# Optimization experiments

Hardware: AMD Instinct MI355X
Metric: run time of the kernel (lower is better)

The kernel has to match this reference:

```python
import jax, jax.numpy as jnp
import numpy as np

N = 100000      # nodes (10000 graphs of 10 nodes)
E = 1600000     # directed edges
IN, H1, H2, H3 = 128, 128, 128, 64
L1, L2, FINAL = 512, 256, 8
K = 2


def lrelu(x, slope):
    return jnp.where(x >= 0, x, slope * x)


def _with_self_loops(edge_index, n):
    loop = jnp.arange(n, dtype=edge_index.dtype)
    src = jnp.concatenate([edge_index[0], loop])
    dst = jnp.concatenate([edge_index[1], loop])
    return src, dst


def _gcn_norm(src, dst, n):
    # symmetric normalization deg^-1/2[src] * deg^-1/2[dst] (self-loops included)
    deg = jax.ops.segment_sum(jnp.ones_like(src, dtype=jnp.float32), dst, num_segments=n)
    dinv = jnp.where(deg > 0, jax.lax.rsqrt(deg), 0.0)
    return dinv[src] * dinv[dst]


def sgconv(x, src, dst, norm, W, b, k_hops):
    # SGConv: K rounds of normalized sparse propagation, then linear
    for _ in range(k_hops):
        x = jax.ops.segment_sum(norm[:, None] * x[src], dst, num_segments=x.shape[0])
    return x @ W + b


def gatconv(x, src, dst, W, att_src, att_dst, b):
    # single-head PyG GATConv (lin bias=False, negative_slope=0.2, self-loops)
    n = x.shape[0]
    h = x @ W                                   # [N, H3]
    a_s = h @ att_src                           # [N]
    a_d = h @ att_dst                           # [N]
    e = lrelu(a_s[src] + a_d[dst], 0.2)         # [E+N]
    m = jax.ops.segment_max(e, dst, num_segments=n)
    e = jnp.exp(e - m[dst])
    s = jax.ops.segment_sum(e, dst, num_segments=n)
    alpha = e / s[dst]
    out = jax.ops.segment_sum(alpha[:, None] * h[src], dst, num_segments=n)
    return out + b


def setup_inputs() -> dict:
    key = jax.random.key(0)
    ks = jax.random.split(key, 16)

    def w(k, shape, fan_in):
        return (jax.random.normal(k, shape, jnp.float32) / np.sqrt(fan_in)).astype(jnp.float32)

    return {
        "x": jax.random.normal(ks[0], (N, IN), jnp.float32),
        "edge_index": jax.random.randint(ks[1], (2, E), 0, N),
        "W1": w(ks[2], (IN, H1), IN), "b1": jnp.zeros((H1,), jnp.float32),
        "W2": w(ks[3], (H1, H2), H1), "b2": jnp.zeros((H2,), jnp.float32),
        "Wg": w(ks[4], (H2, H3), H2),
        "att_src": w(ks[5], (H3,), H3), "att_dst": w(ks[6], (H3,), H3),
        "bg": jnp.zeros((H3,), jnp.float32),
        "Wl1": w(ks[7], (10 * H3, L1), 10 * H3), "bl1": jnp.zeros((L1,), jnp.float32),
        "Wl2": w(ks[8], (L1, L2), L1), "bl2": jnp.zeros((L2,), jnp.float32),
        "Wl3": w(ks[9], (L2, FINAL), L2), "bl3": jnp.zeros((FINAL,), jnp.float32),
    }


def reference(x, edge_index, W1, b1, W2, b2, Wg, att_src, att_dst, bg,
              Wl1, bl1, Wl2, bl2, Wl3, bl3):
    n = x.shape[0]
    src, dst = _with_self_loops(edge_index, n)
    norm = _gcn_norm(src, dst, n)

    h = sgconv(x, src, dst, norm, W1, b1, K)       # conv1
    h = lrelu(h, 0.1)                              # dropout is identity in eval mode
    h = lrelu(sgconv(h, src, dst, norm, W2, b2, K), 0.1)
    h = lrelu(gatconv(h, src, dst, Wg, att_src, att_dst, bg), 0.1)

    h = h.reshape(n // 10, 10 * H3)                # group 10 nodes per graph
    h = lrelu(h @ Wl1 + bl1, 0.1)
    h = lrelu(h @ Wl2 + bl2, 0.1)
    return h @ Wl3 + bl3
```

## Files before the change

kernel.cpp:

```cpp
#include <hip/hip_runtime.h>

typedef __attribute__((ext_vector_type(8))) short short8;
typedef __attribute__((ext_vector_type(8))) unsigned short ushort8;
typedef __attribute__((ext_vector_type(4))) float floatx4;
typedef __attribute__((ext_vector_type(2))) float floatx2;

#define NBQ  1024
#define NBLK 128

__device__ __forceinline__ float bf2f(unsigned short u) {
    union { unsigned u; float f; } v; v.u = ((unsigned)u) << 16; return v.f;
}
__device__ __forceinline__ float bflo(unsigned u) {
    union { unsigned u; float f; } v; v.u = u << 16; return v.f;
}
__device__ __forceinline__ float bfhi(unsigned u) {
    union { unsigned u; float f; } v; v.u = u & 0xFFFF0000u; return v.f;
}
__device__ __forceinline__ unsigned short f2bf(float f) {
    union { float f; unsigned u; } v; v.f = f;
    unsigned r = v.u + 0x7FFFu + ((v.u >> 16) & 1u);
    return (unsigned short)(r >> 16);
}
__device__ __forceinline__ unsigned pack2bf(float a, float b) {
    return (unsigned)f2bf(a) | ((unsigned)f2bf(b) << 16);
}
__device__ __forceinline__ float lrelu(float x, float s) { return x >= 0.f ? x : s * x; }

#define PK_FP8_LO(a, b, old) __builtin_amdgcn_cvt_pk_fp8_f32((a), (b), (old), false)
#define PK_FP8_HI(a, b, old) __builtin_amdgcn_cvt_pk_fp8_f32((a), (b), (old), true)
#define UPK_FP8_LO(u)        __builtin_amdgcn_cvt_pk_f32_fp8((int)(u), false)
#define UPK_FP8_HI(u)        __builtin_amdgcn_cvt_pk_f32_fp8((int)(u), true)

__global__ __launch_bounds__(256) void cast_scale8(const float* __restrict__ in, const float* __restrict__ dinv,
                                                   unsigned* __restrict__ outp, int nquads) {
    int i = blockIdx.x * 256 + threadIdx.x;
    if (i < nquads) {
        float s = dinv[i >> 5];
        float4 v = *(const float4*)(in + 4 * (size_t)i);
        int w = PK_FP8_LO(v.x * s, v.y * s, 0);
        w = PK_FP8_HI(v.z * s, v.w * s, w);
        outp[i] = (unsigned)w;
    }
}

__global__ __launch_bounds__(256) void cast_bf2fp8(const uint2* __restrict__ in, unsigned* __restrict__ outp,
                                                   int nquads) {
    int i = blockIdx.x * 256 + threadIdx.x;
    if (i < nquads) {
        uint2 v = in[i];
        int w = PK_FP8_LO(bflo(v.x), bfhi(v.x), 0);
        w = PK_FP8_HI(bflo(v.y), bfhi(v.y), w);
        outp[i] = (unsigned)w;
    }
}

__global__ __launch_bounds__(256) void wcast(const float* __restrict__ w0, const float* __restrict__ w1,
                                             const float* __restrict__ w2, const float* __restrict__ w3,
                                             const float* __restrict__ w4, unsigned* __restrict__ outp,
                                             int c0, int c1, int c2, int c3, int c4) {
    int i = blockIdx.x * 256 + threadIdx.x;
    if (i >= c4) return;
    const float* src; int base;
    if      (i < c0) { src = w0; base = 0;  }
    else if (i < c1) { src = w1; base = c0; }
    else if (i < c2) { src = w2; base = c1; }
    else if (i < c3) { src = w3; base = c2; }
    else             { src = w4; base = c3; }
    float2 v = *(const float2*)(src + 2 * (size_t)(i - base));
    outp[i] = pack2bf(v.x, v.y);
}

__global__ __launch_bounds__(256) void hist_k(const int* __restrict__ dst, int* __restrict__ cnt,
                                              int e, int et, int nb) {
    __shared__ int h[NBQ];
    for (int i = threadIdx.x; i < nb; i += 256) h[i] = 0;
    __syncthreads();
    int chunk = (et + NBLK - 1) / NBLK;
    int c0 = blockIdx.x * chunk;
    int c1 = c0 + chunk < et ? c0 + chunk : et;
    for (int i = c0 + (int)threadIdx.x; i < c1; i += 256) {
        int d = (i < e) ? dst[i] : (i - e);
        atomicAdd(&h[d >> 7], 1);
    }
    __syncthreads();
    for (int i = threadIdx.x; i < nb; i += 256) cnt[blockIdx.x * NBQ + i] = h[i];
}

__global__ __launch_bounds__(256) void btot_k(const int* __restrict__ cnt, int* __restrict__ btot, int nb) {
    int b = blockIdx.x * 256 + threadIdx.x;
    if (b >= nb) return;
    int s = 0;
    for (int blk = 0; blk < NBLK; ++blk) s += cnt[blk * NBQ + b];
    btot[b] = s;
}

__global__ __launch_bounds__(256) void bscan_k(const int* __restrict__ btot, int* __restrict__ bbase,
                                               int nb, int et) {
    __shared__ int sd[256];
    int t = threadIdx.x;
    int i0 = t * 4;
    int loc[4]; int s = 0;
    for (int j = 0; j < 4; ++j) { int i = i0 + j; loc[j] = (i < nb) ? btot[i] : 0; s += loc[j]; }
    sd[t] = s; __syncthreads();
    for (int off = 1; off < 256; off <<= 1) {
        int v = (t >= off) ? sd[t - off] : 0;
        __syncthreads();
        sd[t] += v;
        __syncthreads();
    }
    int run = sd[t] - s;
    for (int j = 0; j < 4; ++j) {
        int i = i0 + j;
        if (i < nb) { bbase[i] = run; run += loc[j]; }
    }
    if (t == 255) bbase[nb] = et;
}

__global__ __launch_bounds__(256) void scan_cnt(int* __restrict__ cnt, const int* __restrict__ bbase,
                                                int nb) {
    int b = blockIdx.x * 256 + threadIdx.x;
    if (b >= nb) return;
    int base = bbase[b];
    for (int blk = 0; blk < NBLK; ++blk) {
        int* p = &cnt[blk * NBQ + b];
        int t = *p; *p = base; base += t;
    }
}

__global__ __launch_bounds__(256) void scatter_k(const int* __restrict__ src, const int* __restrict__ dst,
                                                 const int* __restrict__ cnt,
                                                 int* __restrict__ ebuf, int e, int et, int nb) {
    __shared__ int cur[NBQ];
    for (int i = threadIdx.x; i < nb; i += 256) cur[i] = cnt[blockIdx.x * NBQ + i];
    __syncthreads();
    int chunk = (et + NBLK - 1) / NBLK;
    int c0 = blockIdx.x * chunk;
    int c1 = c0 + chunk < et ? c0 + chunk : et;
    for (int i = c0 + (int)threadIdx.x; i < c1; i += 256) {
        int s, d;
        if (i < e) { s = src[i]; d = dst[i]; }
        else       { s = d = i - e; }
        int pos = atomicAdd(&cur[d >> 7], 1);
        ebuf[pos] = s | ((d & 127) << 17);
    }
}

__global__ __launch_bounds__(256) void finalize_k(const int* __restrict__ ebuf, const int* __restrict__ bbase,
                                                  int* __restrict__ offsets, float* __restrict__ dinv,
                                                  int* __restrict__ csr_s, int n, int et) {
    __shared__ int ldeg[128];
    __shared__ int lscan[128];
    __shared__ int cur[128];
    int b = blockIdx.x;
    int n0 = b << 7;
    if (threadIdx.x < 128) ldeg[threadIdx.x] = 0;
    __syncthreads();
    int e0 = bbase[b], e1 = bbase[b + 1];
    for (int i = e0 + (int)threadIdx.x; i < e1; i += 256)
        atomicAdd(&ldeg[(ebuf[i] >> 17) & 127], 1);
    __syncthreads();
    if (threadIdx.x < 128) lscan[threadIdx.x] = ldeg[threadIdx.x];
    __syncthreads();
    for (int off = 1; off < 128; off <<= 1) {
        int v = 0;
        if (threadIdx.x < 128 && (int)threadIdx.x >= off) v = lscan[threadIdx.x - off];
        __syncthreads();
        if (threadIdx.x < 128) lscan[threadIdx.x] += v;
        __syncthreads();
    }
    if (threadIdx.x < 128) {
        int base = e0 + lscan[threadIdx.x] - ldeg[threadIdx.x];
        cur[threadIdx.x] = base;
        int node = n0 + threadIdx.x;
        if (node < n) {
            offsets[node] = base;
            dinv[node] = rsqrtf((float)ldeg[threadIdx.x]);
        }
    }
    if (b == 0 && threadIdx.x == 0) offsets[n] = et;
    __syncthreads();
    for (int i = e0 + (int)threadIdx.x; i < e1; i += 256) {
        int ent = ebuf[i];
        int pos = atomicAdd(&cur[(ent >> 17) & 127], 1);
        csr_s[pos] = ent & 0x1FFFF;
    }
}


#define ACC16F(u) { floatx2 t0_ = UPK_FP8_LO((u).x), t1_ = UPK_FP8_HI((u).x); \
                    a[0] += t0_.x; a[1] += t0_.y; a[2] += t1_.x; a[3] += t1_.y; \
                    t0_ = UPK_FP8_LO((u).y); t1_ = UPK_FP8_HI((u).y); \
                    a[4] += t0_.x; a[5] += t0_.y; a[6] += t1_.x; a[7] += t1_.y; \
                    t0_ = UPK_FP8_LO((u).z); t1_ = UPK_FP8_HI((u).z); \
                    a[8] += t0_.x; a[9] += t0_.y; a[10] += t1_.x; a[11] += t1_.y; \
                    t0_ = UPK_FP8_LO((u).w); t1_ = UPK_FP8_HI((u).w); \
                    a[12] += t0_.x; a[13] += t0_.y; a[14] += t1_.x; a[15] += t1_.y; }

__global__ __launch_bounds__(256) void prop8_kernel(const uint4* __restrict__ xin, const int* __restrict__ offs,
                                                    const int* __restrict__ csr_s, const float* __restrict__ dinv,
                                                    int sq, int out8f, uint4* __restrict__ out8,
                                                    uint4* __restrict__ out16, int n) {
    int node = blockIdx.x * 32 + (threadIdx.x >> 3);
    if (node >= n) return;
    int li = threadIdx.x & 7;
    int beg = offs[node], end = offs[node + 1];
    float a[16];
#pragma unroll
    for (int j = 0; j < 16; ++j) a[j] = 0.f;
    int e = beg;
    for (; e + 1 < end; e += 2) {
        int s0 = csr_s[e];
        int s1 = csr_s[e + 1];
        uint4 u0 = xin[(size_t)s0 * 8 + li];
        uint4 u1 = xin[(size_t)s1 * 8 + li];
        ACC16F(u0); ACC16F(u1);
    }
    if (e < end) {
        int s = csr_s[e];
        uint4 u = xin[(size_t)s * 8 + li];
        ACC16F(u);
    }
    float f = dinv[node];
    if (sq) f *= f;
    if (out8f) {
        int w0 = PK_FP8_LO(a[0] * f, a[1] * f, 0);   w0 = PK_FP8_HI(a[2] * f, a[3] * f, w0);
        int w1 = PK_FP8_LO(a[4] * f, a[5] * f, 0);   w1 = PK_FP8_HI(a[6] * f, a[7] * f, w1);
        int w2 = PK_FP8_LO(a[8] * f, a[9] * f, 0);   w2 = PK_FP8_HI(a[10] * f, a[11] * f, w2);
        int w3 = PK_FP8_LO(a[12] * f, a[13] * f, 0); w3 = PK_FP8_HI(a[14] * f, a[15] * f, w3);
        uint4 o; o.x = (unsigned)w0; o.y = (unsigned)w1; o.z = (unsigned)w2; o.w = (unsigned)w3;
        out8[(size_t)node * 8 + li] = o;
    } else {
        uint4 o1, o2;
        o1.x = pack2bf(a[0] * f, a[1] * f);   o1.y = pack2bf(a[2] * f, a[3] * f);
        o1.z = pack2bf(a[4] * f, a[5] * f);   o1.w = pack2bf(a[6] * f, a[7] * f);
        o2.x = pack2bf(a[8] * f, a[9] * f);   o2.y = pack2bf(a[10] * f, a[11] * f);
        o2.z = pack2bf(a[12] * f, a[13] * f); o2.w = pack2bf(a[14] * f, a[15] * f);
        out16[(size_t)node * 16 + li * 2]     = o1;
        out16[(size_t)node * 16 + li * 2 + 1] = o2;
    }
}


__global__ __launch_bounds__(256) void gemm_mfma(const unsigned short* __restrict__ A,
                                                 const unsigned short* __restrict__ Bw,
                                                 const float* __restrict__ bias, unsigned short* __restrict__ C,
                                                 const float* __restrict__ oscale,
                                                 const float* __restrict__ attS, const float* __restrict__ attD,
                                                 float* __restrict__ oas, float* __restrict__ oad,
                                                 int M, int K, int Nc, float slope, int act) {
    __shared__ __align__(16) unsigned short As[64 * 40];
    __shared__ __align__(16) unsigned short Bs[64 * 40];
    const int tid  = threadIdx.x;
    const int wave = tid >> 6;
    const int lane = tid & 63;
    const int q    = lane >> 4;
    const int r16  = lane & 15;
    const int m0 = blockIdx.x * 64;
    const int n0 = blockIdx.y * 64;

    floatx4 acc0 = {0.f,0.f,0.f,0.f}, acc1 = acc0, acc2 = acc0, acc3 = acc0;

    const int am = tid >> 2;
    const int ak = (tid & 3) * 8;
    const int bk = tid >> 3;
    const int bn = (tid & 7) * 8;
    const int gm = m0 + am;

    ushort8 sva, svb;
    if (gm < M) sva = *(const ushort8*)(A + (size_t)gm * K + ak);
    else        for (int j = 0; j < 8; ++j) sva[j] = 0;
    svb = *(const ushort8*)(Bw + (size_t)bk * Nc + n0 + bn);

    for (int k0 = 0; k0 < K; k0 += 32) {
        *(ushort8*)(&As[am * 40 + ak]) = sva;
        for (int j = 0; j < 8; ++j) Bs[(bn + j) * 40 + bk] = svb[j];
        __syncthreads();
        if (k0 + 32 < K) {
            if (gm < M) sva = *(const ushort8*)(A + (size_t)gm * K + k0 + 32 + ak);
            svb = *(const ushort8*)(Bw + (size_t)(k0 + 32 + bk) * Nc + n0 + bn);
        }
        short8 bfrag = *(const short8*)(&Bs[(wave * 16 + r16) * 40 + q * 8]);
        short8 a0 = *(const short8*)(&As[(r16) * 40 + q * 8]);
        short8 a1 = *(const short8*)(&As[(16 + r16) * 40 + q * 8]);
        short8 a2 = *(const short8*)(&As[(32 + r16) * 40 + q * 8]);
        short8 a3 = *(const short8*)(&As[(48 + r16) * 40 + q * 8]);
        acc0 = __builtin_amdgcn_mfma_f32_16x16x32_bf16(a0, bfrag, acc0, 0, 0, 0);
        acc1 = __builtin_amdgcn_mfma_f32_16x16x32_bf16(a1, bfrag, acc1, 0, 0, 0);
        acc2 = __builtin_amdgcn_mfma_f32_16x16x32_bf16(a2, bfrag, acc2, 0, 0, 0);
        acc3 = __builtin_amdgcn_mfma_f32_16x16x32_bf16(a3, bfrag, acc3, 0, 0, 0);
        __syncthreads();
    }
    int cn = n0 + wave * 16 + r16;
    float bv = bias ? bias[cn] : 0.f;
    floatx4 aa[4] = {acc0, acc1, acc2, acc3};
    float ps[16], pd[16];
    float avs = attS ? attS[cn] : 0.f;
    float avd = attS ? attD[cn] : 0.f;
    for (int ms = 0; ms < 4; ++ms)
        for (int rr = 0; rr < 4; ++rr) {
            int cm = m0 + ms * 16 + q * 4 + rr;
            float v = aa[ms][rr] + bv;
            if (act) v = lrelu(v, slope);
            if (oscale && cm < M) v *= oscale[cm];
            if (cm < M) C[(size_t)cm * Nc + cn] = f2bf(v);
            ps[ms * 4 + rr] = v * avs;
            pd[ms * 4 + rr] = v * avd;
        }
    if (attS) {
        for (int off = 1; off < 16; off <<= 1)
#pragma unroll
            for (int i = 0; i < 16; ++i) {
                ps[i] += __shfl_xor(ps[i], off, 64);
                pd[i] += __shfl_xor(pd[i], off, 64);
            }
        float* sd = (float*)As;
        if (tid < 128) sd[tid] = 0.f;
        __syncthreads();
        if (r16 == 0) {
#pragma unroll
            for (int i = 0; i < 16; ++i) {
                int row = (i >> 2) * 16 + q * 4 + (i & 3);
                atomicAdd(&sd[row], ps[i]);
                atomicAdd(&sd[64 + row], pd[i]);
            }
        }
        __syncthreads();
        if (tid < 64 && m0 + tid < M) {
            oas[m0 + tid] = sd[tid];
            oad[m0 + tid] = sd[64 + tid];
        }
    }
}

__global__ __launch_bounds__(256) void gat_agg(const uint4* __restrict__ hg, const float* __restrict__ a_s,
                                               const float* __restrict__ a_d, const int* __restrict__ offs,
                                               const int* __restrict__ csr_s, const float* __restrict__ bg,
                                               uint4* __restrict__ out, int n) {
    int node = blockIdx.x * 32 + (threadIdx.x >> 3);
    if (node >= n) return;
    int li = threadIdx.x & 7;
    int beg = offs[node], end = offs[node + 1];
    float ad = a_d[node];
    float a0=0.f,a1=0.f,a2=0.f,a3=0.f,a4=0.f,a5=0.f,a6=0.f,a7=0.f, ssum=0.f;
    int e = beg;
    for (; e + 1 < end; e += 2) {
        int s0 = csr_s[e];
        int s1 = csr_s[e + 1];
        float t0 = a_s[s0] + ad;
        float t1 = a_s[s1] + ad;
        uint4 u0 = hg[(size_t)s0 * 8 + li];
        uint4 u1 = hg[(size_t)s1 * 8 + li];
        t0 = t0 < 0.f ? 0.2f * t0 : t0;
        t1 = t1 < 0.f ? 0.2f * t1 : t1;
        float w0 = __expf(t0);
        float w1 = __expf(t1);
        ssum += w0 + w1;
        a0 = fmaf(w0, bflo(u0.x), a0); a1 = fmaf(w0, bfhi(u0.x), a1);
        a2 = fmaf(w0, bflo(u0.y), a2); a3 = fmaf(w0, bfhi(u0.y), a3);
        a4 = fmaf(w0, bflo(u0.z), a4); a5 = fmaf(w0, bfhi(u0.z), a5);
        a6 = fmaf(w0, bflo(u0.w), a6); a7 = fmaf(w0, bfhi(u0.w), a7);
        a0 = fmaf(w1, bflo(u1.x), a0); a1 = fmaf(w1, bfhi(u1.x), a1);
        a2 = fmaf(w1, bflo(u1.y), a2); a3 = fmaf(w1, bfhi(u1.y), a3);
        a4 = fmaf(w1, bflo(u1.z), a4); a5 = fmaf(w1, bfhi(u1.z), a5);
        a6 = fmaf(w1, bflo(u1.w), a6); a7 = fmaf(w1, bfhi(u1.w), a7);
    }
    if (e < end) {
        int s0 = csr_s[e];
        float t0 = a_s[s0] + ad;
        uint4 u0 = hg[(size_t)s0 * 8 + li];
        t0 = t0 < 0.f ? 0.2f * t0 : t0;
        float w0 = __expf(t0);
        ssum += w0;
        a0 = fmaf(w0, bflo(u0.x), a0); a1 = fmaf(w0, bfhi(u0.x), a1);
        a2 = fmaf(w0, bflo(u0.y), a2); a3 = fmaf(w0, bfhi(u0.y), a3);
        a4 = fmaf(w0, bflo(u0.z), a4); a5 = fmaf(w0, bfhi(u0.z), a5);
        a6 = fmaf(w0, bflo(u0.w), a6); a7 = fmaf(w0, bfhi(u0.w), a7);
    }
    float inv = 1.0f / ssum;
    int f0 = li * 8;
    uint4 o;
    o.x = pack2bf(lrelu(a0 * inv + bg[f0 + 0], 0.1f), lrelu(a1 * inv + bg[f0 + 1], 0.1f));
    o.y = pack2bf(lrelu(a2 * inv + bg[f0 + 2], 0.1f), lrelu(a3 * inv + bg[f0 + 3], 0.1f));
    o.z = pack2bf(lrelu(a4 * inv + bg[f0 + 4], 0.1f), lrelu(a5 * inv + bg[f0 + 5], 0.1f));
    o.w = pack2bf(lrelu(a6 * inv + bg[f0 + 6], 0.1f), lrelu(a7 * inv + bg[f0 + 7], 0.1f));
    out[(size_t)node * 8 + li] = o;
}


__global__ __launch_bounds__(256) void final_gemm(const unsigned short* __restrict__ m2, const float* __restrict__ W3,
                                                  const float* __restrict__ b3,
                                                  float* __restrict__ out, int ng) {
    int idx = blockIdx.x * 256 + threadIdx.x;
    if (idx >= ng * 8) return;
    int r = idx >> 3, c = idx & 7;
    float acc = b3[c];
    const unsigned short* row = m2 + (size_t)r * 256;
    for (int k = 0; k < 256; ++k) acc = fmaf(bf2f(row[k]), W3[k * 8 + c], acc);
    out[idx] = acc;
}


extern "C" void kernel_launch(void* const* d_in, const int* in_sizes, int n_in,
                              void* d_out, int out_size, void* d_ws, size_t ws_size,
                              hipStream_t stream) {
    const int N  = in_sizes[0] / 128;
    const int E  = in_sizes[1] / 2;
    const int ET = E + N;
    const int Ng = N / 10;
    const int NB = (N + 127) / 128;

    const float* x    = (const float*)d_in[0];
    const int*   src  = (const int*)d_in[1];
    const int*   dst  = src + E;
    const float* W1   = (const float*)d_in[2];
    const float* b1   = (const float*)d_in[3];
    const float* W2   = (const float*)d_in[4];
    const float* b2   = (const float*)d_in[5];
    const float* Wg   = (const float*)d_in[6];
    const float* atts = (const float*)d_in[7];
    const float* attd = (const float*)d_in[8];
    const float* bg   = (const float*)d_in[9];
    const float* Wl1  = (const float*)d_in[10];
    const float* bl1  = (const float*)d_in[11];
    const float* Wl2  = (const float*)d_in[12];
    const float* bl2  = (const float*)d_in[13];
    const float* Wl3  = (const float*)d_in[14];
    const float* bl3  = (const float*)d_in[15];
    float* out = (float*)d_out;

    const int p1 = in_sizes[2] / 2;
    const int p2 = in_sizes[4] / 2;
    const int p3 = in_sizes[6] / 2;
    const int p4 = in_sizes[10] / 2;
    const int p5 = in_sizes[12] / 2;
    const int c0 = p1, c1 = c0 + p2, c2 = c1 + p3, c3 = c2 + p4, c4 = c3 + p5;

    char* p = (char*)d_ws;
    auto alloc = [&](size_t bytes) { char* r = p; p += (bytes + 255) & ~(size_t)255; return r; };
    unsigned short* xb = (unsigned short*)alloc((size_t)N * 128 * 2);
    unsigned short* A  = (unsigned short*)alloc((size_t)N * 128 * 2);
    unsigned short* Bb = (unsigned short*)alloc((size_t)N * 128 * 2);
    int*   csr_s   = (int*)  alloc((size_t)ET * 4);
    int*   cnt     = (int*)  alloc((size_t)NBLK * NBQ * 4);
    int*   btot    = (int*)  alloc((size_t)(NBQ + 1) * 4);
    int*   bbase   = (int*)  alloc((size_t)(NBQ + 1) * 4);
    float* dinv    = (float*)alloc((size_t)N * 4);
    int*   offsets = (int*)  alloc((size_t)(N + 1) * 4);
    float* a_s     = (float*)alloc((size_t)N * 4);
    float* a_d     = (float*)alloc((size_t)N * 4);
    unsigned short* wb = (unsigned short*)alloc((size_t)c4 * 4);
    int*   ebuf    = (int*)Bb;
    unsigned* x8 = (unsigned*)xb;
    uint4*    a8 = (uint4*)(xb + (size_t)N * 64);

    const unsigned short* W1b  = wb;
    const unsigned short* W2b  = wb + 2 * (size_t)c0;
    const unsigned short* Wgb  = wb + 2 * (size_t)c1;
    const unsigned short* Wl1b = wb + 2 * (size_t)c2;
    const unsigned short* Wl2b = wb + 2 * (size_t)c3;

    const int pgp = (N + 31) / 32;

    hist_k    <<<NBLK, 256, 0, stream>>>(dst, cnt, E, ET, NB);
    btot_k    <<<(NB + 255) / 256, 256, 0, stream>>>(cnt, btot, NB);
    bscan_k   <<<1, 256, 0, stream>>>(btot, bbase, NB, ET);
    scan_cnt  <<<(NB + 255) / 256, 256, 0, stream>>>(cnt, bbase, NB);
    scatter_k <<<NBLK, 256, 0, stream>>>(src, dst, cnt, ebuf, E, ET, NB);
    finalize_k<<<NB, 256, 0, stream>>>(ebuf, bbase, offsets, dinv, csr_s, N, ET);
    wcast     <<<(c4 + 255) / 256, 256, 0, stream>>>(W1, W2, Wg, Wl1, Wl2, (unsigned*)wb, c0, c1, c2, c3, c4);
    cast_scale8<<<(N * 32 + 255) / 256, 256, 0, stream>>>(x, dinv, x8, N * 32);

    prop8_kernel<<<pgp, 256, 0, stream>>>((const uint4*)x8, offsets, csr_s, dinv, 1, 1, a8, nullptr, N);
    prop8_kernel<<<pgp, 256, 0, stream>>>(a8, offsets, csr_s, dinv, 0, 0, nullptr, (uint4*)Bb, N);
    dim3 g1((N + 63) / 64, 2);
    gemm_mfma<<<g1, 256, 0, stream>>>(Bb, W1b, b1, A, dinv, nullptr, nullptr, nullptr, nullptr,
                                      N, 128, 128, 0.1f, 1);
    cast_bf2fp8<<<(N * 32 + 255) / 256, 256, 0, stream>>>((const uint2*)A, x8, N * 32);
    prop8_kernel<<<pgp, 256, 0, stream>>>((const uint4*)x8, offsets, csr_s, dinv, 1, 1, a8, nullptr, N);
    prop8_kernel<<<pgp, 256, 0, stream>>>(a8, offsets, csr_s, dinv, 0, 0, nullptr, (uint4*)A, N);
    gemm_mfma<<<g1, 256, 0, stream>>>(A, W2b, b2, Bb, nullptr, nullptr, nullptr, nullptr, nullptr,
                                      N, 128, 128, 0.1f, 1);
    dim3 g2((N + 63) / 64, 1);
    gemm_mfma<<<g2, 256, 0, stream>>>(Bb, Wgb, nullptr, A, nullptr, atts, attd, a_s, a_d,
                                      N, 128, 64, 0.f, 0);
    gat_agg <<<pgp, 256, 0, stream>>>((const uint4*)A, a_s, a_d, offsets, csr_s, bg, (uint4*)Bb, N);
    dim3 g3((Ng + 63) / 64, 8);
    gemm_mfma<<<g3, 256, 0, stream>>>(Bb, Wl1b, bl1, A, nullptr, nullptr, nullptr, nullptr, nullptr,
                                      Ng, 640, 512, 0.1f, 1);
    dim3 g4((Ng + 63) / 64, 4);
    gemm_mfma<<<g4, 256, 0, stream>>>(A, Wl2b, bl2, Bb, nullptr, nullptr, nullptr, nullptr, nullptr,
                                      Ng, 512, 256, 0.1f, 1);
    final_gemm<<<(Ng * 8 + 255) / 256, 256, 0, stream>>>(Bb, Wl3, bl3, out, Ng);
}
```

Measured before the change: 518.6 us.

## Prepack weights into MFMA fragment layout and widen GEMM N-tile per block

Weights are now cast once into a bf16 layout that matches the MFMA B-fragment register order, so the GEMM loads B fragments straight from global memory and no longer transposes them through shared memory. The A tile is double-buffered in LDS, which removes one barrier per k-step. The kernel is templated on the number of 64-wide N tiles per block, and most GEMMs use two, so each A tile is reused across more output columns and half as many blocks are launched. The cost is more accumulator registers per thread and uncoalesced strided reads in the weight cast kernel.

```diff
diff --git a/kernel.cpp b/kernel.cpp
--- a/kernel.cpp
+++ b/kernel.cpp
@@ -55,20 +55,35 @@
     }
 }
 
-__global__ __launch_bounds__(256) void wcast(const float* __restrict__ w0, const float* __restrict__ w1,
-                                             const float* __restrict__ w2, const float* __restrict__ w3,
-                                             const float* __restrict__ w4, unsigned* __restrict__ outp,
-                                             int c0, int c1, int c2, int c3, int c4) {
+__global__ __launch_bounds__(256) void wcast_frag(const float* __restrict__ w0, const float* __restrict__ w1,
+                                                  const float* __restrict__ w2, const float* __restrict__ w3,
+                                                  const float* __restrict__ w4, unsigned short* __restrict__ outp,
+                                                  int f1, int f2, int f3, int f4, int f5,
+                                                  int e1, int e2, int e3, int e4,
+                                                  int k1, int k2, int k3, int k4, int k5,
+                                                  int n1, int n2, int n3, int n4, int n5) {
     int i = blockIdx.x * 256 + threadIdx.x;
-    if (i >= c4) return;
-    const float* src; int base;
-    if      (i < c0) { src = w0; base = 0;  }
-    else if (i < c1) { src = w1; base = c0; }
-    else if (i < c2) { src = w2; base = c1; }
-    else if (i < c3) { src = w3; base = c2; }
-    else             { src = w4; base = c3; }
-    float2 v = *(const float2*)(src + 2 * (size_t)(i - base));
-    outp[i] = pack2bf(v.x, v.y);
+    if (i >= f5) return;
+    const float* W; int fb, eb, K, Nc;
+    if      (i < f1) { W = w0; fb = 0;  eb = 0;  K = k1; Nc = n1; }
+    else if (i < f2) { W = w1; fb = f1; eb = e1; K = k2; Nc = n2; }
+    else if (i < f3) { W = w2; fb = f2; eb = e2; K = k3; Nc = n3; }
+    else if (i < f4) { W = w3; fb = f3; eb = e3; K = k4; Nc = n4; }
+    else             { W = w4; fb = f4; eb = e4; K = k5; Nc = n5; }
+    int f = i - fb;
+    int lane = f & 63;
+    int wave = (f >> 6) & 3;
+    int rest = f >> 8;
+    int ks = K >> 5;
+    int kt = rest % ks;
+    int ntile = rest / ks;
+    int q = lane >> 4, r16 = lane & 15;
+    int n = ntile * 64 + wave * 16 + r16;
+    int kb = kt * 32 + q * 8;
+    ushort8 o;
+#pragma unroll
+    for (int j = 0; j < 8; ++j) o[j] = f2bf(W[(size_t)(kb + j) * Nc + n]);
+    *(ushort8*)(outp + (size_t)eb + (size_t)f * 8) = o;
 }
 
 __global__ __launch_bounds__(256) void hist_k(const int* __restrict__ dst, int* __restrict__ cnt,
@@ -242,93 +257,120 @@
 }
 
 
+template<int NT>
 __global__ __launch_bounds__(256) void gemm_mfma(const unsigned short* __restrict__ A,
-                                                 const unsigned short* __restrict__ Bw,
+                                                 const unsigned short* __restrict__ Bf,
                                                  const float* __restrict__ bias, unsigned short* __restrict__ C,
                                                  const float* __restrict__ oscale,
                                                  const float* __restrict__ attS, const float* __restrict__ attD,
                                                  float* __restrict__ oas, float* __restrict__ oad,
                                                  int M, int K, int Nc, float slope, int act) {
-    __shared__ __align__(16) unsigned short As[64 * 40];
-    __shared__ __align__(16) unsigned short Bs[64 * 40];
+    __shared__ __align__(16) unsigned short As[2][64 * 40];
     const int tid  = threadIdx.x;
     const int wave = tid >> 6;
     const int lane = tid & 63;
     const int q    = lane >> 4;
     const int r16  = lane & 15;
     const int m0 = blockIdx.x * 64;
-    const int n0 = blockIdx.y * 64;
-
-    floatx4 acc0 = {0.f,0.f,0.f,0.f}, acc1 = acc0, acc2 = acc0, acc3 = acc0;
+    const int ksteps = K >> 5;
+
+    floatx4 acc[NT][4];
+#pragma unroll
+    for (int nt = 0; nt < NT; ++nt)
+#pragma unroll
+        for (int ms = 0; ms < 4; ++ms) acc[nt][ms] = floatx4{0.f, 0.f, 0.f, 0.f};
 
     const int am = tid >> 2;
     const int ak = (tid & 3) * 8;
-    const int bk = tid >> 3;
-    const int bn = (tid & 7) * 8;
     const int gm = m0 + am;
 
-    ushort8 sva, svb;
+    ushort8 sva;
     if (gm < M) sva = *(const ushort8*)(A + (size_t)gm * K + ak);
     else        for (int j = 0; j < 8; ++j) sva[j] = 0;
-    svb = *(const ushort8*)(Bw + (size_t)bk * Nc + n0 + bn);
-
-    for (int k0 = 0; k0 < K; k0 += 32) {
-        *(ushort8*)(&As[am * 40 + ak]) = sva;
-        for (int j = 0; j < 8; ++j) Bs[(bn + j) * 40 + bk] = svb[j];
+
+    const unsigned short* bbase = Bf + ((size_t)wave * 64 + lane) * 8;
+
+    for (int kt = 0; kt < ksteps; ++kt) {
+        unsigned short* as = As[kt & 1];
+        *(ushort8*)(&as[am * 40 + ak]) = sva;
         __syncthreads();
-        if (k0 + 32 < K) {
-            if (gm < M) sva = *(const ushort8*)(A + (size_t)gm * K + k0 + 32 + ak);
-            svb = *(const ushort8*)(Bw + (size_t)(k0 + 32 + bk) * Nc + n0 + bn);
+        if (kt + 1 < ksteps) {
+            if (gm < M) sva = *(const ushort8*)(A + (size_t)gm * K + (kt + 1) * 32 + ak);
         }
-        short8 bfrag = *(const short8*)(&Bs[(wave * 16 + r16) * 40 + q * 8]);
-        short8 a0 = *(const short8*)(&As[(r16) * 40 + q * 8]);
-        short8 a1 = *(const short8*)(&As[(16 + r16) * 40 + q * 8]);
-        short8 a2 = *(const short8*)(&As[(32 + r16) * 40 + q * 8]);
-        short8 a3 = *(const short8*)(&As[(48 + r16) * 40 + q * 8]);
-        acc0 = __builtin_amdgcn_mfma_f32_16x16x32_bf16(a0, bfrag, acc0, 0, 0, 0);
-        acc1 = __builtin_amdgcn_mfma_f32_16x16x32_bf16(a1, bfrag, acc1, 0, 0, 0);
-        acc2 = __builtin_amdgcn_mfma_f32_16x16x32_bf16(a2, bfrag, acc2, 0, 0, 0);
-        acc3 = __builtin_amdgcn_mfma_f32_16x16x32_bf16(a3, bfrag, acc3, 0, 0, 0);
-        __syncthreads();
-    }
-    int cn = n0 + wave * 16 + r16;
-    float bv = bias ? bias[cn] : 0.f;
-    floatx4 aa[4] = {acc0, acc1, acc2, acc3};
-    float ps[16], pd[16];
-    float avs = attS ? attS[cn] : 0.f;
-    float avd = attS ? attD[cn] : 0.f;
-    for (int ms = 0; ms < 4; ++ms)
-        for (int rr = 0; rr < 4; ++rr) {
-            int cm = m0 + ms * 16 + q * 4 + rr;
-            float v = aa[ms][rr] + bv;
-            if (act) v = lrelu(v, slope);
-            if (oscale && cm < M) v *= oscale[cm];
-            if (cm < M) C[(size_t)cm * Nc + cn] = f2bf(v);
-            ps[ms * 4 + rr] = v * avs;
-            pd[ms * 4 + rr] = v * avd;
+        short8 bf[NT];
+#pragma unroll
+        for (int nt = 0; nt < NT; ++nt) {
+            int ntg = blockIdx.y * NT + nt;
+            bf[nt] = *(const short8*)(bbase + (size_t)(ntg * ksteps + kt) * 2048);
         }
-    if (attS) {
-        for (int off = 1; off < 16; off <<= 1)
-#pragma unroll
-            for (int i = 0; i < 16; ++i) {
-                ps[i] += __shfl_xor(ps[i], off, 64);
-                pd[i] += __shfl_xor(pd[i], off, 64);
+        short8 a0 = *(const short8*)(&as[(r16) * 40 + q * 8]);
+        short8 a1 = *(const short8*)(&as[(16 + r16) * 40 + q * 8]);
+        short8 a2 = *(const short8*)(&as[(32 + r16) * 40 + q * 8]);
+        short8 a3 = *(const short8*)(&as[(48 + r16) * 40 + q * 8]);
+#pragma unroll
+        for (int nt = 0; nt < NT; ++nt) {
+            acc[nt][0] = __builtin_amdgcn_mfma_f32_16x16x32_bf16(a0, bf[nt], acc[nt][0], 0, 0, 0);
+            acc[nt][1] = __builtin_amdgcn_mfma_f32_16x16x32_bf16(a1, bf[nt], acc[nt][1], 0, 0, 0);
+            acc[nt][2] = __builtin_amdgcn_mfma_f32_16x16x32_bf16(a2, bf[nt], acc[nt][2], 0, 0, 0);
+            acc[nt][3] = __builtin_amdgcn_mfma_f32_16x16x32_bf16(a3, bf[nt], acc[nt][3], 0, 0, 0);
+        }
+    }
+    if constexpr (NT == 1) {
+        int cn = blockIdx.y * 64 + wave * 16 + r16;
+        float bv = bias ? bias[cn] : 0.f;
+        float ps[16], pd[16];
+        float avs = attS ? attS[cn] : 0.f;
+        float avd = attS ? attD[cn] : 0.f;
+        for (int ms = 0; ms < 4; ++ms)
+            for (int rr = 0; rr < 4; ++rr) {
+                int cm = m0 + ms * 16 + q * 4 + rr;
+                float v = acc[0][ms][rr] + bv;
+                if (act) v = lrelu(v, slope);
+                if (oscale && cm < M) v *= oscale[cm];
+                if (cm < M) C[(size_t)cm * Nc + cn] = f2bf(v);
+                ps[ms * 4 + rr] = v * avs;
+                pd[ms * 4 + rr] = v * avd;
             }
-        float* sd = (float*)As;
-        if (tid < 128) sd[tid] = 0.f;
-        __syncthreads();
-        if (r16 == 0) {
-#pragma unroll
-            for (int i = 0; i < 16; ++i) {
-                int row = (i >> 2) * 16 + q * 4 + (i & 3);
-                atomicAdd(&sd[row], ps[i]);
-                atomicAdd(&sd[64 + row], pd[i]);
+        if (attS) {
+            for (int off = 1; off < 16; off <<= 1)
+#pragma unroll
+                for (int i = 0; i < 16; ++i) {
+                    ps[i] += __shfl_xor(ps[i], off, 64);
+                    pd[i] += __shfl_xor(pd[i], off, 64);
+                }
+            __syncthreads();
+            float* sd = (float*)As[0];
+            if (tid < 128) sd[tid] = 0.f;
+            __syncthreads();
+            if (r16 == 0) {
+#pragma unroll
+                for (int i = 0; i < 16; ++i) {
+                    int row = (i >> 2) * 16 + q * 4 + (i & 3);
+                    atomicAdd(&sd[row], ps[i]);
+                    atomicAdd(&sd[64 + row], pd[i]);
+                }
+            }
+            __syncthreads();
+            if (tid < 64 && m0 + tid < M) {
+                oas[m0 + tid] = sd[tid];
+                oad[m0 + tid] = sd[64 + tid];
             }
         }
-        __syncthreads();
-        if (tid < 64 && m0 + tid < M) {
-            oas[m0 + tid] = sd[tid];
-            oad[m0 + tid] = sd[64 + tid];
+    } else {
+#pragma unroll
+        for (int nt = 0; nt < NT; ++nt) {
+            int cn = blockIdx.y * (NT * 64) + nt * 64 + wave * 16 + r16;
+            float bv = bias ? bias[cn] : 0.f;
+#pragma unroll
+            for (int ms = 0; ms < 4; ++ms)
+#pragma unroll
+                for (int rr = 0; rr < 4; ++rr) {
+                    int cm = m0 + ms * 16 + q * 4 + rr;
+                    float v = acc[nt][ms][rr] + bv;
+                    if (act) v = lrelu(v, slope);
+                    if (oscale && cm < M) v *= oscale[cm];
+                    if (cm < M) C[(size_t)cm * Nc + cn] = f2bf(v);
+                }
         }
     }
 }
@@ -429,12 +471,15 @@
     const float* bl3  = (const float*)d_in[15];
     float* out = (float*)d_out;
 
-    const int p1 = in_sizes[2] / 2;
-    const int p2 = in_sizes[4] / 2;
-    const int p3 = in_sizes[6] / 2;
-    const int p4 = in_sizes[10] / 2;
-    const int p5 = in_sizes[12] / 2;
-    const int c0 = p1, c1 = c0 + p2, c2 = c1 + p3, c3 = c2 + p4, c4 = c3 + p5;
+    const int K1 = 128,     N1 = in_sizes[2]  / K1;
+    const int K2 = N1,      N2 = in_sizes[4]  / K2;
+    const int K3 = N2,      N3 = in_sizes[6]  / K3;
+    const int K4 = 10 * N3, N4 = in_sizes[10] / K4;
+    const int K5 = N4,      N5 = in_sizes[12] / K5;
+    const int F1 = K1 * N1 / 8,      F2 = F1 + K2 * N2 / 8, F3 = F2 + K3 * N3 / 8;
+    const int F4 = F3 + K4 * N4 / 8, F5 = F4 + K5 * N5 / 8;
+    const int E1 = K1 * N1, E2 = E1 + K2 * N2, E3 = E2 + K3 * N3, E4 = E3 + K4 * N4;
+    const int ET5 = E4 + K5 * N5;
 
     char* p = (char*)d_ws;
     auto alloc = [&](size_t bytes) { char* r = p; p += (bytes + 255) & ~(size_t)255; return r; };
@@ -449,16 +494,16 @@
     int*   offsets = (int*)  alloc((size_t)(N + 1) * 4);
     float* a_s     = (float*)alloc((size_t)N * 4);
     float* a_d     = (float*)alloc((size_t)N * 4);
-    unsigned short* wb = (unsigned short*)alloc((size_t)c4 * 4);
+    unsigned short* wb = (unsigned short*)alloc((size_t)ET5 * 2);
     int*   ebuf    = (int*)Bb;
     unsigned* x8 = (unsigned*)xb;
     uint4*    a8 = (uint4*)(xb + (size_t)N * 64);
 
     const unsigned short* W1b  = wb;
-    const unsigned short* W2b  = wb + 2 * (size_t)c0;
-    const unsigned short* Wgb  = wb + 2 * (size_t)c1;
-    const unsigned short* Wl1b = wb + 2 * (size_t)c2;
-    const unsigned short* Wl2b = wb + 2 * (size_t)c3;
+    const unsigned short* W2b  = wb + E1;
+    const unsigned short* Wgb  = wb + E2;
+    const unsigned short* Wl1b = wb + E3;
+    const unsigned short* Wl2b = wb + E4;
 
     const int pgp = (N + 31) / 32;
 
@@ -468,28 +513,30 @@
     scan_cnt  <<<(NB + 255) / 256, 256, 0, stream>>>(cnt, bbase, NB);
     scatter_k <<<NBLK, 256, 0, stream>>>(src, dst, cnt, ebuf, E, ET, NB);
     finalize_k<<<NB, 256, 0, stream>>>(ebuf, bbase, offsets, dinv, csr_s, N, ET);
-    wcast     <<<(c4 + 255) / 256, 256, 0, stream>>>(W1, W2, Wg, Wl1, Wl2, (unsigned*)wb, c0, c1, c2, c3, c4);
+    wcast_frag<<<(F5 + 255) / 256, 256, 0, stream>>>(W1, W2, Wg, Wl1, Wl2, wb,
+                                                     F1, F2, F3, F4, F5, E1, E2, E3, E4,
+                                                     K1, K2, K3, K4, K5, N1, N2, N3, N4, N5);
     cast_scale8<<<(N * 32 + 255) / 256, 256, 0, stream>>>(x, dinv, x8, N * 32);
 
     prop8_kernel<<<pgp, 256, 0, stream>>>((const uint4*)x8, offsets, csr_s, dinv, 1, 1, a8, nullptr, N);
     prop8_kernel<<<pgp, 256, 0, stream>>>(a8, offsets, csr_s, dinv, 0, 0, nullptr, (uint4*)Bb, N);
-    dim3 g1((N + 63) / 64, 2);
-    gemm_mfma<<<g1, 256, 0, stream>>>(Bb, W1b, b1, A, dinv, nullptr, nullptr, nullptr, nullptr,
-                                      N, 128, 128, 0.1f, 1);
+    dim3 g1((N + 63) / 64, 1);
+    gemm_mfma<2><<<g1, 256, 0, stream>>>(Bb, W1b, b1, A, dinv, nullptr, nullptr, nullptr, nullptr,
+                                         N, 128, 128, 0.1f, 1);
     cast_bf2fp8<<<(N * 32 + 255) / 256, 256, 0, stream>>>((const uint2*)A, x8, N * 32);
     prop8_kernel<<<pgp, 256, 0, stream>>>((const uint4*)x8, offsets, csr_s, dinv, 1, 1, a8, nullptr, N);
     prop8_kernel<<<pgp, 256, 0, stream>>>(a8, offsets, csr_s, dinv, 0, 0, nullptr, (uint4*)A, N);
-    gemm_mfma<<<g1, 256, 0, stream>>>(A, W2b, b2, Bb, nullptr, nullptr, nullptr, nullptr, nullptr,
-                                      N, 128, 128, 0.1f, 1);
+    gemm_mfma<2><<<g1, 256, 0, stream>>>(A, W2b, b2, Bb, nullptr, nullptr, nullptr, nullptr, nullptr,
+                                         N, 128, 128, 0.1f, 1);
     dim3 g2((N + 63) / 64, 1);
-    gemm_mfma<<<g2, 256, 0, stream>>>(Bb, Wgb, nullptr, A, nullptr, atts, attd, a_s, a_d,
-                                      N, 128, 64, 0.f, 0);
+    gemm_mfma<1><<<g2, 256, 0, stream>>>(Bb, Wgb, nullptr, A, nullptr, atts, attd, a_s, a_d,
+                                         N, 128, 64, 0.f, 0);
     gat_agg <<<pgp, 256, 0, stream>>>((const uint4*)A, a_s, a_d, offsets, csr_s, bg, (uint4*)Bb, N);
-    dim3 g3((Ng + 63) / 64, 8);
-    gemm_mfma<<<g3, 256, 0, stream>>>(Bb, Wl1b, bl1, A, nullptr, nullptr, nullptr, nullptr, nullptr,
-                                      Ng, 640, 512, 0.1f, 1);
-    dim3 g4((Ng + 63) / 64, 4);
-    gemm_mfma<<<g4, 256, 0, stream>>>(A, Wl2b, bl2, Bb, nullptr, nullptr, nullptr, nullptr, nullptr,
-                                      Ng, 512, 256, 0.1f, 1);
+    dim3 g3((Ng + 63) / 64, 4);
+    gemm_mfma<2><<<g3, 256, 0, stream>>>(Bb, Wl1b, bl1, A, nullptr, nullptr, nullptr, nullptr, nullptr,
+                                         Ng, 640, 512, 0.1f, 1);
+    dim3 g4((Ng + 63) / 64, 2);
+    gemm_mfma<2><<<g4, 256, 0, stream>>>(A, Wl2b, bl2, Bb, nullptr, nullptr, nullptr, nullptr, nullptr,
+                                         Ng, 512, 256, 0.1f, 1);
     final_gemm<<<(Ng * 8 + 255) / 256, 256, 0, stream>>>(Bb, Wl3, bl3, out, Ng);
 }
```

After: 475.7 us. -8.3%, faster.
